# Kernel tuning notes

Hardware: AMD Instinct MI355X
Metric: run time of the kernel (lower is better)

The kernel has to match this reference:

```python
import jax, jax.numpy as jnp
import numpy as np

N_B, N_A = 32, 48
H_IN, E_IN, H_H, H_G, NCELLS = 64, 32, 64, 16, 5


def setup_inputs() -> dict:
    key = jax.random.key(0)
    ks = jax.random.split(key, 10)
    A = (jax.random.uniform(ks[0], (N_B, N_A, N_A)) < 0.3).astype(jnp.float32)
    h = jax.random.normal(ks[1], (N_B, N_A, H_IN), dtype=jnp.float32)
    E = jax.random.normal(ks[2], (N_B, N_A, N_A, E_IN), dtype=jnp.float32)
    s_h = 1.0 / np.sqrt(H_IN)
    s_e = 1.0 / np.sqrt(E_IN)
    s_g = 1.0 / np.sqrt(H_H)
    W_h = jax.random.uniform(ks[3], (H_IN, H_H), minval=-s_h, maxval=s_h)
    b_h = jax.random.uniform(ks[4], (H_H,), minval=-s_h, maxval=s_h)
    W_e = jax.random.uniform(ks[5], (E_IN, H_G * H_H), minval=-s_e, maxval=s_e)
    b_e = jax.random.uniform(ks[6], (H_G * H_H,), minval=-s_e, maxval=s_e)
    W_ih = jax.random.uniform(ks[7], (3 * H_H, H_G), minval=-s_g, maxval=s_g)
    W_hh = jax.random.uniform(ks[8], (3 * H_H, H_H), minval=-s_g, maxval=s_g)
    b_ih = jax.random.uniform(jax.random.fold_in(key, 11), (3 * H_H,), minval=-s_g, maxval=s_g)
    b_hh = jax.random.uniform(jax.random.fold_in(key, 12), (3 * H_H,), minval=-s_g, maxval=s_g)
    return {"A": A, "h": h, "E": E, "W_h": W_h, "b_h": b_h, "W_e": W_e, "b_e": b_e,
            "W_ih": W_ih, "b_ih": b_ih, "W_hh": W_hh, "b_hh": b_hh}


def _gru_cell(x, hprev, W_ih, b_ih, W_hh, b_hh):
    # PyTorch GRUCell semantics
    gi = x @ W_ih.T + b_ih      # [N, 3*H_H]
    gh = hprev @ W_hh.T + b_hh  # [N, 3*H_H]
    i_r, i_z, i_n = jnp.split(gi, 3, axis=-1)
    h_r, h_z, h_n = jnp.split(gh, 3, axis=-1)
    r = jax.nn.sigmoid(i_r + h_r)
    z = jax.nn.sigmoid(i_z + h_z)
    n = jnp.tanh(i_n + r * h_n)
    return (1.0 - z) * n + z * hprev


def reference(A, h, E, W_h, b_h, W_e, b_e, W_ih, b_ih, W_hh, b_hh):
    N_b, n_a = h.shape[0], A.shape[1]
    maskh = (jnp.sum(A, axis=-1, keepdims=True) > 0.1).astype(jnp.float32)  # [B,n,1]
    hv = jax.nn.relu(h @ W_h + b_h) * maskh                                 # [B,n,H_H]
    Ee = jax.nn.relu(E @ W_e + b_e).reshape(N_b, n_a, n_a, H_G, H_H)
    Ee = Ee * A[..., None, None]                                            # mask edges
    # E.matmul(h).sum(dim=1) == (sum_i E[b,i,j]) @ h[b,j]; precompute the i-sum
    Esum = Ee.sum(axis=1)                                                   # [B,j,G,H]
    hc = hv  # [B,n,H_H]
    for _ in range(NCELLS):
        M = jnp.einsum('bjgh,bjh->bjg', Esum, hc).reshape(N_b * n_a, H_G)
        hc = _gru_cell(M, hc.reshape(N_b * n_a, H_H), W_ih, b_ih, W_hh, b_hh)
        hc = hc.reshape(N_b, n_a, H_H)
    return hc
```

## Files before the change

### kernel.cpp

```cpp
#include <hip/hip_runtime.h>
#include <stdint.h>

#define NB 32
#define NA 48
#define HIN 64
#define EIN 32
#define HH 64
#define HG 16
#define NCELLS 5
#define GH 1024
#define EROW 40
#define P3 3
#define ESTR 1088

typedef __attribute__((ext_vector_type(8))) short short8;
typedef __attribute__((ext_vector_type(4))) float float4v;

__device__ __forceinline__ unsigned short f2bf(float f) {
    union { float f; unsigned int u; } v; v.f = f;
    unsigned int u = v.u + 0x7FFF + ((v.u >> 16) & 1);
    return (unsigned short)(u >> 16);
}
__device__ __forceinline__ float bf2f(unsigned short s) {
    union { unsigned int u; float f; } v; v.u = ((unsigned int)s) << 16;
    return v.f;
}

__global__ __launch_bounds__(256) void prep(const float* __restrict__ W_e,
                                            const float* __restrict__ W_ih,
                                            const float* __restrict__ W_hh,
                                            unsigned short* __restrict__ hiB,
                                            unsigned short* __restrict__ loB,
                                            float4* __restrict__ gw4) {
    const int idx = blockIdx.x * 256 + threadIdx.x;
    if (idx < 32768) {
        const int ct = idx >> 9, l = (idx >> 3) & 63, jj = idx & 7;
        const int k = (l >> 4) * 8 + jj;
        const int c = ct * 16 + (l & 15);
        const float x = W_e[k * GH + c];
        const unsigned short hb = f2bf(x);
        hiB[idx] = hb;
        loB[idx] = f2bf(x - bf2f(hb));
    } else {
        const int o = idx - 32768;
        if (o < 20 * 192) {
            const int j = o / 192, c = o - j * 192;
            float4 v;
            if (j < 4)  v = *(const float4*)(W_ih + c * HG + 4 * j);
            else        v = *(const float4*)(W_hh + c * HH + 4 * (j - 4));
            gw4[o] = v;
        }
    }
}

template <int NTMAX>
__device__ __forceinline__ void edge_phase3(
    const unsigned short* __restrict__ hiB, const unsigned short* __restrict__ loB,
    const float* __restrict__ b_e,
    const unsigned short* EcolH, const unsigned short* EcolL,
    const float* mask_s,
    int wave, int lane, int mrow, int quad,
    float* Esum_s)
{
    const float4v zero4 = {0.0f, 0.0f, 0.0f, 0.0f};
    short8 aH[P3][NTMAX ? NTMAX : 1], aL[P3][NTMAX ? NTMAX : 1];
    #pragma unroll
    for (int p = 0; p < P3; ++p)
        #pragma unroll
        for (int rt = 0; rt < NTMAX; ++rt) {
            const int off = (p * 48 + 16 * rt + mrow) * EROW + quad * 8;
            aH[p][rt] = *(const short8*)(EcolH + off);
            aL[p][rt] = *(const short8*)(EcolL + off);
        }

    #pragma unroll 4
    for (int t = 0; t < 16; ++t) {
        const int ct = wave * 16 + t;
        const short8 bfH = *(const short8*)(hiB + (size_t)ct * 512 + lane * 8);
        const short8 bfL = *(const short8*)(loB + (size_t)ct * 512 + lane * 8);
        const float be = b_e[ct * 16 + mrow];
        float psum[P3] = {0.0f, 0.0f, 0.0f};
        #pragma unroll
        for (int p = 0; p < P3; ++p) {
            #pragma unroll
            for (int rt = 0; rt < NTMAX; ++rt) {
                float4v d = __builtin_amdgcn_mfma_f32_16x16x32_bf16(aL[p][rt], bfH, zero4, 0, 0, 0);
                d = __builtin_amdgcn_mfma_f32_16x16x32_bf16(aH[p][rt], bfL, d, 0, 0, 0);
                d = __builtin_amdgcn_mfma_f32_16x16x32_bf16(aH[p][rt], bfH, d, 0, 0, 0);
                const float4v mk = *(const float4v*)(mask_s + p * 48 + rt * 16 + quad * 4);
                #pragma unroll
                for (int rg = 0; rg < 4; ++rg)
                    psum[p] = fmaf(fmaxf(d[rg] + be, 0.0f), mk[rg], psum[p]);
            }
        }
        #pragma unroll
        for (int p = 0; p < P3; ++p) {
            float ps = psum[p];
            ps += __shfl_xor(ps, 16);
            ps += __shfl_xor(ps, 32);
            if (lane < 16) {
                const int c = ct * 16 + lane;
                Esum_s[p * ESTR + (c >> 6) * 68 + (c & 63)] = ps;
            }
        }
    }
}

__global__ __launch_bounds__(256, 2) void fused_kernel(
    const float* __restrict__ A,  const float* __restrict__ h,
    const float* __restrict__ E,
    const float* __restrict__ W_h, const float* __restrict__ b_h,
    const float* __restrict__ b_e,
    const float* __restrict__ b_ih, const float* __restrict__ b_hh,
    const unsigned short* __restrict__ hiB, const unsigned short* __restrict__ loB,
    const float4* __restrict__ gw4,
    float* __restrict__ out)
{
    __shared__ unsigned short EcolH[P3 * NA * EROW];
    __shared__ unsigned short EcolL[P3 * NA * EROW];
    __shared__ float Esum_s[P3 * ESTR];
    __shared__ float mask_s[P3 * 48];
    __shared__ int   ilist[P3 * NA];
    __shared__ int   cnt_s[P3];
    __shared__ float hc_s[P3 * HH];
    __shared__ float M_s[P3 * HG];
    __shared__ float gsum_s[P3 * 2 * HH];
    __shared__ float gin_s[P3 * HH], ghn_s[P3 * HH];

    const int node0 = blockIdx.x * P3;
    const int b = node0 / NA, j0 = node0 - b * NA;
    const int tid = threadIdx.x, lane = tid & 63, wave = tid >> 6;
    const int mrow = lane & 15, quad = lane >> 4;

    if (wave < P3) {
        const float a = (lane < NA) ? A[((size_t)b * NA + lane) * NA + (j0 + wave)] : 0.0f;
        const unsigned long long m = __ballot(a != 0.0f);
        if (a != 0.0f) ilist[wave * NA + __popcll(m & ((1ull << lane) - 1ull))] = lane;
        if (lane == 0) cnt_s[wave] = (int)__popcll(m);
    }
    __syncthreads();

    for (int idx = tid; idx < P3 * NA * 8; idx += 256) {
        const int p = idx / (NA * 8);
        const int rem = idx - p * (NA * 8);
        const int r = rem >> 3, q = rem & 7;
        uint2 hv2 = make_uint2(0u, 0u), lv2 = make_uint2(0u, 0u);
        if (r < cnt_s[p]) {
            const int i = ilist[p * NA + r];
            const float4 ev = *(const float4*)(E + ((size_t)(b * NA + i) * NA + (j0 + p)) * EIN + 4 * q);
            unsigned short h0 = f2bf(ev.x), h1 = f2bf(ev.y), h2 = f2bf(ev.z), h3 = f2bf(ev.w);
            unsigned short l0 = f2bf(ev.x - bf2f(h0)), l1 = f2bf(ev.y - bf2f(h1));
            unsigned short l2 = f2bf(ev.z - bf2f(h2)), l3 = f2bf(ev.w - bf2f(h3));
            hv2 = make_uint2((unsigned int)h0 | ((unsigned int)h1 << 16),
                             (unsigned int)h2 | ((unsigned int)h3 << 16));
            lv2 = make_uint2((unsigned int)l0 | ((unsigned int)l1 << 16),
                             (unsigned int)l2 | ((unsigned int)l3 << 16));
        }
        *(uint2*)(&EcolH[(p * NA + r) * EROW + 4 * q]) = hv2;
        *(uint2*)(&EcolL[(p * NA + r) * EROW + 4 * q]) = lv2;
    }
    if (tid < P3 * 48) {
        const int p = tid / 48, rem = tid - p * 48;
        mask_s[tid] = (rem < cnt_s[p]) ? 1.0f : 0.0f;
    }
    __syncthreads();

    const int nt0 = (cnt_s[0] + 15) >> 4, nt1 = (cnt_s[1] + 15) >> 4, nt2 = (cnt_s[2] + 15) >> 4;
    int ntmax = nt0 > nt1 ? nt0 : nt1; ntmax = ntmax > nt2 ? ntmax : nt2;

    if (ntmax == 0)
        edge_phase3<0>(hiB, loB, b_e, EcolH, EcolL, mask_s, wave, lane, mrow, quad, Esum_s);
    else if (ntmax == 1)
        edge_phase3<1>(hiB, loB, b_e, EcolH, EcolL, mask_s, wave, lane, mrow, quad, Esum_s);
    else if (ntmax == 2)
        edge_phase3<2>(hiB, loB, b_e, EcolH, EcolL, mask_s, wave, lane, mrow, quad, Esum_s);
    else
        edge_phase3<3>(hiB, loB, b_e, EcolH, EcolL, mask_s, wave, lane, mrow, quad, Esum_s);

    float bihc = 0.0f, bhhc = 0.0f;
    if (tid < 3 * HH) { bihc = b_ih[tid]; bhhc = b_hh[tid]; }

    if (wave < P3) {
        const int node = node0 + wave;
        const float a = (lane < NA) ? A[(size_t)node * NA + lane] : 0.0f;
        const unsigned long long mrowm = __ballot(a != 0.0f);
        const float maskh = (mrowm != 0ull) ? 1.0f : 0.0f;
        const float hr = h[(size_t)node * HIN + lane];
        float acc = b_h[lane];
        #pragma unroll
        for (int k = 0; k < HIN; ++k)
            acc = fmaf(__shfl(hr, k), W_h[k * HH + lane], acc);
        hc_s[wave * HH + lane] = fmaxf(acc, 0.0f) * maskh;
    }
    __syncthreads();

    #pragma unroll 1
    for (int it = 0; it < NCELLS; ++it) {
        if (tid < 192) {
            const int p = tid >> 6, s = tid & 63, g = s >> 2, q = s & 3;
            const float* ep = Esum_s + p * ESTR + g * 68 + q * 16;
            const float* hp = hc_s + p * HH + q * 16;
            const float4v e0 = *(const float4v*)(ep),     h0 = *(const float4v*)(hp);
            const float4v e1 = *(const float4v*)(ep + 4), h1 = *(const float4v*)(hp + 4);
            const float4v e2 = *(const float4v*)(ep + 8), h2 = *(const float4v*)(hp + 8);
            const float4v e3 = *(const float4v*)(ep + 12), h3 = *(const float4v*)(hp + 12);
            float pp = e0[0] * h0[0];
            pp = fmaf(e0[1], h0[1], pp); pp = fmaf(e0[2], h0[2], pp); pp = fmaf(e0[3], h0[3], pp);
            pp = fmaf(e1[0], h1[0], pp); pp = fmaf(e1[1], h1[1], pp);
            pp = fmaf(e1[2], h1[2], pp); pp = fmaf(e1[3], h1[3], pp);
            pp = fmaf(e2[0], h2[0], pp); pp = fmaf(e2[1], h2[1], pp);
            pp = fmaf(e2[2], h2[2], pp); pp = fmaf(e2[3], h2[3], pp);
            pp = fmaf(e3[0], h3[0], pp); pp = fmaf(e3[1], h3[1], pp);
            pp = fmaf(e3[2], h3[2], pp); pp = fmaf(e3[3], h3[3], pp);
            pp += __shfl_xor(pp, 1);
            pp += __shfl_xor(pp, 2);
            if (q == 0) M_s[p * HG + g] = pp;
        }
        __syncthreads();
        if (tid < 192) {
            const float4* gp = gw4 + tid;
            float gi0 = bihc, gi1 = bihc, gi2 = bihc;
            #pragma unroll
            for (int jj = 0; jj < 4; ++jj) {
                const float4 w = gp[jj * 192];
                const float4v m0 = *(const float4v*)(M_s + 0 * HG + 4 * jj);
                const float4v m1 = *(const float4v*)(M_s + 1 * HG + 4 * jj);
                const float4v m2 = *(const float4v*)(M_s + 2 * HG + 4 * jj);
                gi0 = fmaf(m0[0], w.x, gi0); gi0 = fmaf(m0[1], w.y, gi0);
                gi0 = fmaf(m0[2], w.z, gi0); gi0 = fmaf(m0[3], w.w, gi0);
                gi1 = fmaf(m1[0], w.x, gi1); gi1 = fmaf(m1[1], w.y, gi1);
                gi1 = fmaf(m1[2], w.z, gi1); gi1 = fmaf(m1[3], w.w, gi1);
                gi2 = fmaf(m2[0], w.x, gi2); gi2 = fmaf(m2[1], w.y, gi2);
                gi2 = fmaf(m2[2], w.z, gi2); gi2 = fmaf(m2[3], w.w, gi2);
            }
            float gh0 = bhhc, gh1 = bhhc, gh2 = bhhc;
            #pragma unroll
            for (int jj = 4; jj < 20; ++jj) {
                const float4 w = gp[jj * 192];
                const float4v h0 = *(const float4v*)(hc_s + 0 * HH + 4 * (jj - 4));
                const float4v h1 = *(const float4v*)(hc_s + 1 * HH + 4 * (jj - 4));
                const float4v h2 = *(const float4v*)(hc_s + 2 * HH + 4 * (jj - 4));
                gh0 = fmaf(h0[0], w.x, gh0); gh0 = fmaf(h0[1], w.y, gh0);
                gh0 = fmaf(h0[2], w.z, gh0); gh0 = fmaf(h0[3], w.w, gh0);
                gh1 = fmaf(h1[0], w.x, gh1); gh1 = fmaf(h1[1], w.y, gh1);
                gh1 = fmaf(h1[2], w.z, gh1); gh1 = fmaf(h1[3], w.w, gh1);
                gh2 = fmaf(h2[0], w.x, gh2); gh2 = fmaf(h2[1], w.y, gh2);
                gh2 = fmaf(h2[2], w.z, gh2); gh2 = fmaf(h2[3], w.w, gh2);
            }
            if (tid < 2 * HH) {
                gsum_s[0 * 2 * HH + tid] = gi0 + gh0;
                gsum_s[1 * 2 * HH + tid] = gi1 + gh1;
                gsum_s[2 * 2 * HH + tid] = gi2 + gh2;
            } else {
                const int c = tid - 2 * HH;
                gin_s[0 * HH + c] = gi0; ghn_s[0 * HH + c] = gh0;
                gin_s[1 * HH + c] = gi1; ghn_s[1 * HH + c] = gh1;
                gin_s[2 * HH + c] = gi2; ghn_s[2 * HH + c] = gh2;
            }
        }
        __syncthreads();
        if (tid < 192) {
            const int p = tid >> 6, c = tid & 63;
            const float r = 1.0f / (1.0f + __expf(-gsum_s[p * 2 * HH + c]));
            const float z = 1.0f / (1.0f + __expf(-gsum_s[p * 2 * HH + HH + c]));
            const float nin = gin_s[p * HH + c] + r * ghn_s[p * HH + c];
            const float n = 1.0f - 2.0f / (__expf(2.0f * nin) + 1.0f);
            hc_s[p * HH + c] = (1.0f - z) * n + z * hc_s[p * HH + c];
        }
        __syncthreads();
    }

    if (tid < 192) out[(size_t)node0 * HH + tid] = hc_s[tid];
}

extern "C" void kernel_launch(void* const* d_in, const int* in_sizes, int n_in,
                              void* d_out, int out_size, void* d_ws, size_t ws_size,
                              hipStream_t stream) {
    const float* A    = (const float*)d_in[0];
    const float* h    = (const float*)d_in[1];
    const float* E    = (const float*)d_in[2];
    const float* W_h  = (const float*)d_in[3];
    const float* b_h  = (const float*)d_in[4];
    const float* W_e  = (const float*)d_in[5];
    const float* b_e  = (const float*)d_in[6];
    const float* W_ih = (const float*)d_in[7];
    const float* b_ih = (const float*)d_in[8];
    const float* W_hh = (const float*)d_in[9];
    const float* b_hh = (const float*)d_in[10];
    unsigned short* hiB = (unsigned short*)d_ws;
    unsigned short* loB = hiB + 32768;
    float4* gw4 = (float4*)(loB + 32768);
    float* out = (float*)d_out;

    hipLaunchKernelGGL(prep, dim3(144), dim3(256), 0, stream,
                       W_e, W_ih, W_hh, hiB, loB, gw4);
    hipLaunchKernelGGL(fused_kernel, dim3(NB * NA / P3), dim3(256), 0, stream,
                       A, h, E, W_h, b_h, b_e, b_ih, b_hh, hiB, loB, gw4, out);
}
```

Measured before the change: 102.7 us.

## Fold weight prep into fused kernel and cache GRU weights in registers

Removes the separate prep launch. Each block now converts W_e to bf16 hi/lo pairs on the fly while building the MFMA B fragments, instead of reading precomputed arrays from the workspace. The GRU input and hidden weights are loaded once per thread into a 20-element float4 register array rather than read from global memory each cell, and the trailing barrier in the GRU loop is dropped because each wave only touches its own node between the remaining barriers. The trade-offs are redundant W_e conversion work and global reads in every block, plus much higher register pressure under a two-blocks-per-SM launch bound.

```diff
diff --git a/kernel.cpp b/kernel.cpp
--- a/kernel.cpp
+++ b/kernel.cpp
@@ -26,37 +26,9 @@
     return v.f;
 }
 
-__global__ __launch_bounds__(256) void prep(const float* __restrict__ W_e,
-                                            const float* __restrict__ W_ih,
-                                            const float* __restrict__ W_hh,
-                                            unsigned short* __restrict__ hiB,
-                                            unsigned short* __restrict__ loB,
-                                            float4* __restrict__ gw4) {
-    const int idx = blockIdx.x * 256 + threadIdx.x;
-    if (idx < 32768) {
-        const int ct = idx >> 9, l = (idx >> 3) & 63, jj = idx & 7;
-        const int k = (l >> 4) * 8 + jj;
-        const int c = ct * 16 + (l & 15);
-        const float x = W_e[k * GH + c];
-        const unsigned short hb = f2bf(x);
-        hiB[idx] = hb;
-        loB[idx] = f2bf(x - bf2f(hb));
-    } else {
-        const int o = idx - 32768;
-        if (o < 20 * 192) {
-            const int j = o / 192, c = o - j * 192;
-            float4 v;
-            if (j < 4)  v = *(const float4*)(W_ih + c * HG + 4 * j);
-            else        v = *(const float4*)(W_hh + c * HH + 4 * (j - 4));
-            gw4[o] = v;
-        }
-    }
-}
-
 template <int NTMAX>
 __device__ __forceinline__ void edge_phase3(
-    const unsigned short* __restrict__ hiB, const unsigned short* __restrict__ loB,
-    const float* __restrict__ b_e,
+    const float* __restrict__ W_e, const float* __restrict__ b_e,
     const unsigned short* EcolH, const unsigned short* EcolL,
     const float* mask_s,
     int wave, int lane, int mrow, int quad,
@@ -76,8 +48,14 @@
     #pragma unroll 4
     for (int t = 0; t < 16; ++t) {
         const int ct = wave * 16 + t;
-        const short8 bfH = *(const short8*)(hiB + (size_t)ct * 512 + lane * 8);
-        const short8 bfL = *(const short8*)(loB + (size_t)ct * 512 + lane * 8);
+        short8 bfH, bfL;
+        #pragma unroll
+        for (int jj = 0; jj < 8; ++jj) {
+            const float x = W_e[(quad * 8 + jj) * GH + ct * 16 + mrow];
+            const unsigned short hb = f2bf(x);
+            bfH[jj] = (short)hb;
+            bfL[jj] = (short)f2bf(x - bf2f(hb));
+        }
         const float be = b_e[ct * 16 + mrow];
         float psum[P3] = {0.0f, 0.0f, 0.0f};
         #pragma unroll
@@ -110,10 +88,9 @@
     const float* __restrict__ A,  const float* __restrict__ h,
     const float* __restrict__ E,
     const float* __restrict__ W_h, const float* __restrict__ b_h,
-    const float* __restrict__ b_e,
-    const float* __restrict__ b_ih, const float* __restrict__ b_hh,
-    const unsigned short* __restrict__ hiB, const unsigned short* __restrict__ loB,
-    const float4* __restrict__ gw4,
+    const float* __restrict__ W_e, const float* __restrict__ b_e,
+    const float* __restrict__ W_ih, const float* __restrict__ b_ih,
+    const float* __restrict__ W_hh, const float* __restrict__ b_hh,
     float* __restrict__ out)
 {
     __shared__ unsigned short EcolH[P3 * NA * EROW];
@@ -169,13 +146,13 @@
     int ntmax = nt0 > nt1 ? nt0 : nt1; ntmax = ntmax > nt2 ? ntmax : nt2;
 
     if (ntmax == 0)
-        edge_phase3<0>(hiB, loB, b_e, EcolH, EcolL, mask_s, wave, lane, mrow, quad, Esum_s);
+        edge_phase3<0>(W_e, b_e, EcolH, EcolL, mask_s, wave, lane, mrow, quad, Esum_s);
     else if (ntmax == 1)
-        edge_phase3<1>(hiB, loB, b_e, EcolH, EcolL, mask_s, wave, lane, mrow, quad, Esum_s);
+        edge_phase3<1>(W_e, b_e, EcolH, EcolL, mask_s, wave, lane, mrow, quad, Esum_s);
     else if (ntmax == 2)
-        edge_phase3<2>(hiB, loB, b_e, EcolH, EcolL, mask_s, wave, lane, mrow, quad, Esum_s);
+        edge_phase3<2>(W_e, b_e, EcolH, EcolL, mask_s, wave, lane, mrow, quad, Esum_s);
     else
-        edge_phase3<3>(hiB, loB, b_e, EcolH, EcolL, mask_s, wave, lane, mrow, quad, Esum_s);
+        edge_phase3<3>(W_e, b_e, EcolH, EcolL, mask_s, wave, lane, mrow, quad, Esum_s);
 
     float bihc = 0.0f, bhhc = 0.0f;
     if (tid < 3 * HH) { bihc = b_ih[tid]; bhhc = b_hh[tid]; }
@@ -191,6 +168,17 @@
         for (int k = 0; k < HIN; ++k)
             acc = fmaf(__shfl(hr, k), W_h[k * HH + lane], acc);
         hc_s[wave * HH + lane] = fmaxf(acc, 0.0f) * maskh;
+    }
+
+    __builtin_amdgcn_sched_barrier(0);
+    float4 w_r[20];
+    if (tid < 192) {
+        #pragma unroll
+        for (int j = 0; j < 4; ++j)
+            w_r[j] = *(const float4*)(W_ih + tid * HG + 4 * j);
+        #pragma unroll
+        for (int j = 0; j < 16; ++j)
+            w_r[4 + j] = *(const float4*)(W_hh + tid * HH + 4 * j);
     }
     __syncthreads();
 
@@ -218,11 +206,10 @@
         }
         __syncthreads();
         if (tid < 192) {
-            const float4* gp = gw4 + tid;
             float gi0 = bihc, gi1 = bihc, gi2 = bihc;
             #pragma unroll
             for (int jj = 0; jj < 4; ++jj) {
-                const float4 w = gp[jj * 192];
+                const float4 w = w_r[jj];
                 const float4v m0 = *(const float4v*)(M_s + 0 * HG + 4 * jj);
                 const float4v m1 = *(const float4v*)(M_s + 1 * HG + 4 * jj);
                 const float4v m2 = *(const float4v*)(M_s + 2 * HG + 4 * jj);
@@ -236,7 +223,7 @@
             float gh0 = bhhc, gh1 = bhhc, gh2 = bhhc;
             #pragma unroll
             for (int jj = 4; jj < 20; ++jj) {
-                const float4 w = gp[jj * 192];
+                const float4 w = w_r[jj];
                 const float4v h0 = *(const float4v*)(hc_s + 0 * HH + 4 * (jj - 4));
                 const float4v h1 = *(const float4v*)(hc_s + 1 * HH + 4 * (jj - 4));
                 const float4v h2 = *(const float4v*)(hc_s + 2 * HH + 4 * (jj - 4));
@@ -267,7 +254,6 @@
             const float n = 1.0f - 2.0f / (__expf(2.0f * nin) + 1.0f);
             hc_s[p * HH + c] = (1.0f - z) * n + z * hc_s[p * HH + c];
         }
-        __syncthreads();
     }
 
     if (tid < 192) out[(size_t)node0 * HH + tid] = hc_s[tid];
@@ -287,13 +273,9 @@
     const float* b_ih = (const float*)d_in[8];
     const float* W_hh = (const float*)d_in[9];
     const float* b_hh = (const float*)d_in[10];
-    unsigned short* hiB = (unsigned short*)d_ws;
-    unsigned short* loB = hiB + 32768;
-    float4* gw4 = (float4*)(loB + 32768);
     float* out = (float*)d_out;
-
-    hipLaunchKernelGGL(prep, dim3(144), dim3(256), 0, stream,
-                       W_e, W_ih, W_hh, hiB, loB, gw4);
+    (void)d_ws; (void)ws_size;
+
     hipLaunchKernelGGL(fused_kernel, dim3(NB * NA / P3), dim3(256), 0, stream,
-                       A, h, E, W_h, b_h, b_e, b_ih, b_hh, hiB, loB, gw4, out);
-}
+                       A, h, E, W_h, b_h, W_e, b_e, W_ih, b_ih, W_hh, b_hh, out);
+}
```

Measured after the change: 105.4 us. +2.6%, slower.
